# Kernel optimization log

Hardware: AMD Instinct MI355X
Metric: run time of the kernel (lower is better)

The kernel has to match this reference:

```python
import jax, jax.numpy as jnp
import numpy as np
from jax import lax

IN_CH = 192
CENTER_CH = 192
MID_CH = 192
K = 3
BS, H, W = 8, 64, 64
MASK_NUM = 16


def conv2d(x, w, b, padding=0, groups=1):
    # x: (N,C,H,W), w: (O, I/groups, kh, kw)
    out = lax.conv_general_dilated(
        x, w, window_strides=(1, 1),
        padding=[(padding, padding), (padding, padding)],
        dimension_numbers=('NCHW', 'OIHW', 'NCHW'),
        feature_group_count=groups)
    return out + b[None, :, None, None]


def lrelu(x):
    return jax.nn.leaky_relu(x, negative_slope=0.1)


def setup_inputs() -> dict:
    key = jax.random.key(0)
    ks = jax.random.split(key, 32)
    s = 0.02
    d = {
        'input': jax.random.normal(ks[0], (BS, IN_CH, H, W), jnp.float32),
        'list_center': jax.random.normal(ks[1], (BS, MASK_NUM, CENTER_CH), jnp.float32),
        'batch_mask': jax.random.randint(ks[2], (BS, H, W), 0, MASK_NUM),
        # self.conv: conv1x1(in,mid) -> lrelu -> conv1x1(mid,mid)
        'w0': jax.random.normal(ks[3], (MID_CH, IN_CH, 1, 1)) * s,
        'b0': jnp.zeros((MID_CH,)),
        'w1': jax.random.normal(ks[4], (MID_CH, MID_CH, 1, 1)) * s,
        'b1': jnp.zeros((MID_CH,)),
        # k_sp_gen: conv1x1(mid+center,mid), 3x3(mid,mid), depthwise 3x3(mid -> mid*k^2, groups=mid)
        'ws0': jax.random.normal(ks[5], (MID_CH, MID_CH + CENTER_CH, 1, 1)) * s,
        'bs0': jnp.zeros((MID_CH,)),
        'ws1': jax.random.normal(ks[6], (MID_CH, MID_CH, K, K)) * s,
        'bs1': jnp.zeros((MID_CH,)),
        'ws2': jax.random.normal(ks[7], (MID_CH * K * K, 1, K, K)) * s,
        'bs2': jnp.zeros((MID_CH * K * K,)),
        # k_ch_gen: GAP -> conv1x1 -> lrelu -> conv1x1 -> sigmoid
        'wc0': jax.random.normal(ks[8], (MID_CH, MID_CH, 1, 1)) * s,
        'bc0': jnp.zeros((MID_CH,)),
        'wc1': jax.random.normal(ks[9], (MID_CH, MID_CH, 1, 1)) * s,
        'bc1': jnp.zeros((MID_CH,)),
        # conv_out
        'wo': jax.random.normal(ks[10], (IN_CH, MID_CH, 1, 1)) * s,
        'bo': jnp.zeros((IN_CH,)),
    }
    return d


def mask_expand(list_center, batch_mask):
    # list_center: (bs, mask_num, ch); batch_mask: (bs, h, w) int
    # -> (bs, ch, h, w)
    gathered = jax.vmap(lambda c, m: c[m])(list_center, batch_mask)  # (bs,h,w,ch)
    return jnp.transpose(gathered, (0, 3, 1, 2))


def dynamic_conv(x, k_sp, k):
    # x: (bs, ch, h, w); k_sp: (bs, ch, k^2, h, w)
    bs, ch, h, w = x.shape
    p = (k - 1) // 2
    xp = jnp.pad(x, ((0, 0), (0, 0), (p, p), (p, p)))
    # torch Unfold ordering: kernel index = ki*k + kj, channel-major in view
    patches = jnp.stack([xp[:, :, i:i + h, j:j + w]
                         for i in range(k) for j in range(k)], axis=2)
    return jnp.einsum('bckhw,bckhw->bchw', patches, k_sp)


def reference(input, list_center, batch_mask, w0, b0, w1, b1, ws0, bs0,
              ws1, bs1, ws2, bs2, wc0, bc0, wc1, bc1, wo, bo):
    bs, _, h, w = input.shape
    k = K
    ch = MID_CH
    centers_exp = mask_expand(list_center, batch_mask)  # (bs, center_ch, h, w)
    shortcut = input
    x = conv2d(lrelu(conv2d(input, w0, b0)), w1, b1)  # self.conv
    y = jnp.concatenate([x, centers_exp], axis=1)
    y = lrelu(conv2d(y, ws0, bs0))
    y = lrelu(conv2d(y, ws1, bs1, padding=(k - 1) // 2))
    k_sp = conv2d(y, ws2, bs2, padding=(k - 1) // 2, groups=ch)
    k_sp = k_sp.reshape(bs, ch, k * k, h, w)
    out = dynamic_conv(x, k_sp, k)
    # squeeze-excite channel gate
    g = jnp.mean(out, axis=(2, 3), keepdims=True)
    g = jax.nn.sigmoid(conv2d(lrelu(conv2d(g, wc0, bc0)), wc1, bc1))
    out = g * out
    out = conv2d(out, wo, bo)
    return out + shortcut
```

## Files before the change

### kernel.cpp

```cpp
#include <hip/hip_runtime.h>
#include <hip/hip_bf16.h>

#define CH   192
#define PIX  4096
#define BSZ  8

using f32x4  = __attribute__((ext_vector_type(4))) float;
using short8 = __attribute__((ext_vector_type(8))) short;

__device__ __forceinline__ float bf2f(unsigned short u) {
    union { unsigned u32; float f; } x; x.u32 = ((unsigned)u) << 16; return x.f;
}
__device__ __forceinline__ unsigned short f2bf(float f) {
    union { float f; unsigned u; } x; x.f = f;
    unsigned u = x.u;
    unsigned r = (u + 0x7FFFu + ((u >> 16) & 1u)) >> 16;
    return (unsigned short)r;
}

__device__ __forceinline__ short8 ldsBs(const unsigned short* B, int ST, int k0, int px) {
    short8 f;
    #pragma unroll
    for (int e = 0; e < 8; ++e) f[e] = (short)B[(k0 + e) * ST + px];
    return f;
}

__global__ void k_prep_w(const float* __restrict__ w0, const float* __restrict__ w1,
                         const float* __restrict__ ws0, const float* __restrict__ wo,
                         const float* __restrict__ ws1,
                         unsigned short* __restrict__ w0f, unsigned short* __restrict__ w1f,
                         unsigned short* __restrict__ ws0xf, unsigned short* __restrict__ wof,
                         unsigned short* __restrict__ wc3f, float* __restrict__ gsum) {
    int i = blockIdx.x * 256 + threadIdx.x;
    if (i < 4*36864) {
        int which = i / 36864, j = i % 36864;
        int kc = j / 6144, r = j % 6144, mf = r / 512, r2 = r % 512;
        int l = r2 >> 3, e = r2 & 7;
        int o = mf*16 + (l & 15), k = kc*32 + ((l >> 4) << 3) + e;
        float v;
        unsigned short* dst;
        if (which == 0)      { v = w0[o*192 + k];  dst = w0f;   }
        else if (which == 1) { v = w1[o*192 + k];  dst = w1f;   }
        else if (which == 2) { v = ws0[o*384 + k]; dst = ws0xf; }
        else                 { v = wo[o*192 + k];  dst = wof;   }
        dst[j] = f2bf(v);
        return;
    }
    i -= 4*36864;
    if (i < 331776) {
        int tk = i / 6144, tap = tk / 6, kc = tk % 6;
        int r = i % 6144, mf = r / 512, r2 = r % 512;
        int l = r2 >> 3, e = r2 & 7;
        int o = mf*16 + (l & 15), c = kc*32 + ((l >> 4) << 3) + e;
        wc3f[i] = f2bf(ws1[(o*192 + c)*9 + tap]);
        return;
    }
    i -= 331776;
    if (i < 1536) gsum[i] = 0.f;
}

__global__ void k_tcent(const float* __restrict__ ws0, const float* __restrict__ lc,
                        float* __restrict__ tc) {
    int m = blockIdx.x, b = blockIdx.y, o = threadIdx.x;
    __shared__ float cbuf[192];
    cbuf[o] = lc[(b*16 + m)*192 + o];
    __syncthreads();
    float a = 0.f;
    const float* wr = ws0 + o*384 + 192;
    for (int c = 0; c < 192; ++c) a += wr[c] * cbuf[c];
    tc[(b*16 + m)*192 + o] = a;
}

__global__ __launch_bounds__(256) void k_fused3(
    const float* __restrict__ input,
    const unsigned short* __restrict__ w0f,
    const unsigned short* __restrict__ w1f,
    const unsigned short* __restrict__ ws0xf,
    const float* __restrict__ b0, const float* __restrict__ b1,
    const float* __restrict__ bs0,
    const float* __restrict__ tc, const int* __restrict__ mask,
    unsigned short* __restrict__ xg, unsigned short* __restrict__ y0t)
{
    const int b = blockIdx.y, n0 = blockIdx.x * 64;
    __shared__ unsigned short Bsm[192*66];
    __shared__ unsigned short Csm[192*67];
    const int tid = threadIdx.x, lane = tid & 63, wv = tid >> 6;
    const int li = lane & 15, kq = lane >> 4;

    {
        const float* src = input + (size_t)b*192*PIX + n0;
        #pragma unroll
        for (int j = 0; j < 6; ++j) {
            int q = tid + 256*j, k = q >> 3, g = (q & 7)*8;
            float4 v0 = *(const float4*)(src + (size_t)k*PIX + g);
            float4 v1 = *(const float4*)(src + (size_t)k*PIX + g + 4);
            unsigned d0 = f2bf(v0.x) | ((unsigned)f2bf(v0.y) << 16);
            unsigned d1 = f2bf(v0.z) | ((unsigned)f2bf(v0.w) << 16);
            unsigned d2 = f2bf(v1.x) | ((unsigned)f2bf(v1.y) << 16);
            unsigned d3 = f2bf(v1.z) | ((unsigned)f2bf(v1.w) << 16);
            unsigned* d = (unsigned*)(Bsm + k*66 + g);
            d[0]=d0; d[1]=d1; d[2]=d2; d[3]=d3;
        }
    }
    __syncthreads();

    f32x4 acc[3][4];

    #pragma unroll
    for (int m = 0; m < 3; ++m)
        #pragma unroll
        for (int n = 0; n < 4; ++n) acc[m][n] = {0.f,0.f,0.f,0.f};
    for (int kc = 0; kc < 6; ++kc) {
        short8 a[3];
        #pragma unroll
        for (int m = 0; m < 3; ++m)
            a[m] = *(const short8*)(w0f + ((kc*12 + wv*3 + m)*64 + lane)*8);
        #pragma unroll
        for (int n = 0; n < 4; ++n) {
            short8 fb = ldsBs(Bsm, 66, kc*32 + kq*8, n*16 + li);
            #pragma unroll
            for (int m = 0; m < 3; ++m)
                acc[m][n] = __builtin_amdgcn_mfma_f32_16x16x32_bf16(a[m], fb, acc[m][n], 0,0,0);
        }
    }
    #pragma unroll
    for (int m = 0; m < 3; ++m) {
        int o0 = (wv*3 + m)*16 + kq*4;
        #pragma unroll
        for (int n = 0; n < 4; ++n) {
            int px = n*16 + li;
            #pragma unroll
            for (int r = 0; r < 4; ++r) {
                float v = acc[m][n][r] + b0[o0 + r];
                v = v > 0.f ? v : 0.1f*v;
                Csm[(o0 + r)*67 + px] = f2bf(v);
            }
        }
    }
    __syncthreads();

    #pragma unroll
    for (int m = 0; m < 3; ++m)
        #pragma unroll
        for (int n = 0; n < 4; ++n) acc[m][n] = {0.f,0.f,0.f,0.f};
    for (int kc = 0; kc < 6; ++kc) {
        short8 a[3];
        #pragma unroll
        for (int m = 0; m < 3; ++m)
            a[m] = *(const short8*)(w1f + ((kc*12 + wv*3 + m)*64 + lane)*8);
        #pragma unroll
        for (int n = 0; n < 4; ++n) {
            short8 fb = ldsBs(Csm, 67, kc*32 + kq*8, n*16 + li);
            #pragma unroll
            for (int m = 0; m < 3; ++m)
                acc[m][n] = __builtin_amdgcn_mfma_f32_16x16x32_bf16(a[m], fb, acc[m][n], 0,0,0);
        }
    }
    __syncthreads();
    #pragma unroll
    for (int m = 0; m < 3; ++m) {
        int o0 = (wv*3 + m)*16 + kq*4;
        #pragma unroll
        for (int n = 0; n < 4; ++n) {
            int px = n*16 + li;
            #pragma unroll
            for (int r = 0; r < 4; ++r) {
                float v = acc[m][n][r] + b1[o0 + r];
                unsigned short h = f2bf(v);
                Bsm[(o0 + r)*66 + px] = h;
                xg[((size_t)b*192 + o0 + r)*PIX + n0 + px] = h;
            }
        }
    }
    __syncthreads();

    #pragma unroll
    for (int m = 0; m < 3; ++m)
        #pragma unroll
        for (int n = 0; n < 4; ++n) acc[m][n] = {0.f,0.f,0.f,0.f};
    for (int kc = 0; kc < 6; ++kc) {
        short8 a[3];
        #pragma unroll
        for (int m = 0; m < 3; ++m)
            a[m] = *(const short8*)(ws0xf + ((kc*12 + wv*3 + m)*64 + lane)*8);
        #pragma unroll
        for (int n = 0; n < 4; ++n) {
            short8 fb = ldsBs(Bsm, 66, kc*32 + kq*8, n*16 + li);
            #pragma unroll
            for (int m = 0; m < 3; ++m)
                acc[m][n] = __builtin_amdgcn_mfma_f32_16x16x32_bf16(a[m], fb, acc[m][n], 0,0,0);
        }
    }
    int mi_[4];
    #pragma unroll
    for (int n = 0; n < 4; ++n) mi_[n] = mask[b*PIX + n0 + n*16 + li];
    #pragma unroll
    for (int m = 0; m < 3; ++m) {
        int o0 = (wv*3 + m)*16 + kq*4;
        #pragma unroll
        for (int n = 0; n < 4; ++n) {
            int px = n*16 + li;
            const float* tcb = tc + (b*16 + mi_[n])*192;
            ushort4 w;
            unsigned short* wp = (unsigned short*)&w;
            #pragma unroll
            for (int r = 0; r < 4; ++r) {
                float v = acc[m][n][r] + bs0[o0 + r] + tcb[o0 + r];
                v = v > 0.f ? v : 0.1f*v;
                wp[r] = f2bf(v);
            }
            *(ushort4*)(Csm + px*200 + o0) = w;
        }
    }
    __syncthreads();
    #pragma unroll
    for (int j = 0; j < 6; ++j) {
        int u = tid + 256*j;
        int px = u / 24, chunk = u % 24;
        uint4 v = *(const uint4*)(Csm + px*200 + chunk*8);
        *(uint4*)(y0t + ((size_t)(b*4096 + n0 + px))*192 + chunk*8) = v;
    }
}

__global__ __launch_bounds__(512) void k_conv3t(
    const unsigned short* __restrict__ wc3f,
    const unsigned short* __restrict__ y0t,
    const float* __restrict__ bias,
    unsigned short* __restrict__ y1)
{
    const int b = blockIdx.y, h = blockIdx.x;
    __shared__ unsigned short Bs[3*66*40];
    const int tid = threadIdx.x, lane = tid & 63, wv = tid >> 6;
    const int li = lane & 15, kq = lane >> 4;
    const int mw = wv >> 1, nh = wv & 1;

    f32x4 acc[3][2];
    #pragma unroll
    for (int m = 0; m < 3; ++m)
        #pragma unroll
        for (int nn = 0; nn < 2; ++nn) acc[m][nn] = {0.f,0.f,0.f,0.f};

    for (int kc = 0; kc < 6; ++kc) {
        for (int u = tid; u < 792; u += 512) {
            int row = u >> 2, chunk = u & 3;
            int dr = row / 66, pxl = row % 66;
            int hh = h + dr - 1, pxg = pxl - 1;
            uint4 v = {0u,0u,0u,0u};
            if ((unsigned)hh < 64u && (unsigned)pxg < 64u)
                v = *(const uint4*)(y0t + ((size_t)(b*4096 + hh*64 + pxg))*192 + kc*32 + chunk*8);
            *(uint4*)((char*)Bs + row*80 + chunk*16) = v;
        }
        __syncthreads();

        #pragma unroll
        for (int tap = 0; tap < 9; ++tap) {
            const int dr = tap / 3, dc1 = tap % 3;
            short8 a[3];
            #pragma unroll
            for (int m = 0; m < 3; ++m)
                a[m] = *(const short8*)(wc3f + (((tap*6 + kc)*12 + mw*3 + m)*64 + lane)*8);
            #pragma unroll
            for (int nn = 0; nn < 2; ++nn) {
                int pxi = nh*32 + nn*16 + li + dc1;
                short8 fb = *(const short8*)((const char*)Bs + (dr*66 + pxi)*80 + kq*16);
                #pragma unroll
                for (int m = 0; m < 3; ++m)
                    acc[m][nn] = __builtin_amdgcn_mfma_f32_16x16x32_bf16(a[m], fb, acc[m][nn], 0,0,0);
            }
        }
        __syncthreads();
    }

    #pragma unroll
    for (int m = 0; m < 3; ++m) {
        int o0 = (mw*3 + m)*16 + kq*4;
        #pragma unroll
        for (int nn = 0; nn < 2; ++nn) {
            int px = h*64 + nh*32 + nn*16 + li;
            #pragma unroll
            for (int r = 0; r < 4; ++r) {
                float v = acc[m][nn][r] + bias[o0 + r];
                v = v > 0.f ? v : 0.1f*v;
                y1[((size_t)b*192 + o0 + r)*PIX + px] = f2bf(v);
            }
        }
    }
}

__global__ __launch_bounds__(256) void k_dwdyn2(
    const unsigned short* __restrict__ Y1,
    const unsigned short* __restrict__ X,
    const float* __restrict__ ws2,
    const float* __restrict__ bs2,
    unsigned short* __restrict__ OP,
    float* __restrict__ gsum)
{
    const int c = blockIdx.x, b = blockIdx.y;
    __shared__ unsigned short ysm[4096];
    __shared__ unsigned short xsm[4096];
    __shared__ float wsm[81], bsm9[9], red[4];
    const int tid = threadIdx.x;
    const size_t cb = ((size_t)b*192 + c) * PIX;
    #pragma unroll
    for (int j = 0; j < 2; ++j) {
        int i = tid + 256*j;
        *(uint4*)(ysm + i*8) = *(const uint4*)(Y1 + cb + i*8);
        *(uint4*)(xsm + i*8) = *(const uint4*)(X  + cb + i*8);
    }
    if (tid < 81) wsm[tid] = ws2[c*81 + tid];
    else if (tid < 90) bsm9[tid-81] = bs2[c*9 + tid - 81];
    __syncthreads();

    float gacc = 0.f;
    for (int i = 0; i < 16; ++i) {
        int px = tid + 256*i, hh = px >> 6, ww = px & 63;
        float ksp[9];
        #pragma unroll
        for (int j = 0; j < 9; ++j) ksp[j] = bsm9[j];
        #pragma unroll
        for (int tap = 0; tap < 9; ++tap) {
            int h2 = hh + tap/3 - 1, w2 = ww + tap%3 - 1;
            float yv = ((unsigned)h2 < 64u && (unsigned)w2 < 64u)
                       ? bf2f(ysm[h2*64 + w2]) : 0.f;
            #pragma unroll
            for (int j = 0; j < 9; ++j) ksp[j] += yv * wsm[j*9 + tap];
        }
        float out = 0.f;
        #pragma unroll
        for (int j = 0; j < 9; ++j) {
            int h2 = hh + j/3 - 1, w2 = ww + j%3 - 1;
            float xv = ((unsigned)h2 < 64u && (unsigned)w2 < 64u)
                       ? bf2f(xsm[h2*64 + w2]) : 0.f;
            out += xv * ksp[j];
        }
        OP[cb + px] = f2bf(out);
        gacc += out;
    }
    #pragma unroll
    for (int off = 32; off > 0; off >>= 1) gacc += __shfl_down(gacc, off);
    if ((tid & 63) == 0) red[tid >> 6] = gacc;
    __syncthreads();
    if (tid == 0) gsum[b*192 + c] = red[0] + red[1] + red[2] + red[3];
}

__global__ void k_gate(const float* __restrict__ gsum,
                       const float* __restrict__ wc0, const float* __restrict__ bc0,
                       const float* __restrict__ wc1, const float* __restrict__ bc1,
                       float* __restrict__ gvec)
{
    const int b = blockIdx.x, t = threadIdx.x;
    __shared__ float mean[192], s1[192];
    mean[t] = gsum[b*192 + t] * (1.f/4096.f);
    __syncthreads();
    float a = bc0[t];
    const float* w = wc0 + t*192;
    for (int i = 0; i < 192; ++i) a += w[i] * mean[i];
    s1[t] = a > 0.f ? a : 0.1f * a;
    __syncthreads();
    float a2 = bc1[t];
    const float* w2 = wc1 + t*192;
    for (int i = 0; i < 192; ++i) a2 += w2[i] * s1[i];
    gvec[b*192 + t] = 1.f / (1.f + __expf(-a2));
}

__global__ __launch_bounds__(256) void k_gemmo(
    const unsigned short* __restrict__ wof,
    const unsigned short* __restrict__ op,
    const float* __restrict__ bo,
    const float* __restrict__ gvec,
    const float* __restrict__ resid,
    float* __restrict__ out)
{
    const int b = blockIdx.y, n0 = blockIdx.x * 64;
    __shared__ unsigned short Bsm[192*66];
    const int tid = threadIdx.x, lane = tid & 63, wv = tid >> 6;
    const int li = lane & 15, kq = lane >> 4;

    {
        const unsigned short* src = op + (size_t)b*192*PIX + n0;
        #pragma unroll
        for (int j = 0; j < 6; ++j) {
            int q = tid + 256*j, k = q >> 3, g = (q & 7) * 8;
            uint4 v = *(const uint4*)(src + (size_t)k*PIX + g);
            float gs = gvec[b*192 + k];
            unsigned short* pv = (unsigned short*)&v;
            #pragma unroll
            for (int e = 0; e < 8; ++e) pv[e] = f2bf(bf2f(pv[e]) * gs);
            unsigned* d = (unsigned*)(Bsm + k*66 + g);
            const unsigned* s = (const unsigned*)&v;
            d[0]=s[0]; d[1]=s[1]; d[2]=s[2]; d[3]=s[3];
        }
    }
    __syncthreads();

    f32x4 acc[3][4];
    #pragma unroll
    for (int m = 0; m < 3; ++m)
        #pragma unroll
        for (int n = 0; n < 4; ++n) acc[m][n] = {0.f,0.f,0.f,0.f};
    for (int kc = 0; kc < 6; ++kc) {
        short8 a[3];
        #pragma unroll
        for (int m = 0; m < 3; ++m)
            a[m] = *(const short8*)(wof + ((kc*12 + wv*3 + m)*64 + lane)*8);
        #pragma unroll
        for (int n = 0; n < 4; ++n) {
            short8 fb = ldsBs(Bsm, 66, kc*32 + kq*8, n*16 + li);
            #pragma unroll
            for (int m = 0; m < 3; ++m)
                acc[m][n] = __builtin_amdgcn_mfma_f32_16x16x32_bf16(a[m], fb, acc[m][n], 0,0,0);
        }
    }
    #pragma unroll
    for (int m = 0; m < 3; ++m) {
        int o0 = (wv*3 + m)*16 + kq*4;
        #pragma unroll
        for (int n = 0; n < 4; ++n) {
            int px = n*16 + li;
            #pragma unroll
            for (int r = 0; r < 4; ++r) {
                size_t idx = ((size_t)b*192 + o0 + r)*PIX + n0 + px;
                out[idx] = acc[m][n][r] + bo[o0 + r] + resid[idx];
            }
        }
    }
}

extern "C" void kernel_launch(void* const* d_in, const int* in_sizes, int n_in,
                              void* d_out, int out_size, void* d_ws, size_t ws_size,
                              hipStream_t stream)
{
    const float* input = (const float*)d_in[0];
    const float* lc    = (const float*)d_in[1];
    const int*   mask  = (const int*)d_in[2];
    const float* w0  = (const float*)d_in[3];
    const float* b0  = (const float*)d_in[4];
    const float* w1  = (const float*)d_in[5];
    const float* b1  = (const float*)d_in[6];
    const float* ws0 = (const float*)d_in[7];
    const float* bs0 = (const float*)d_in[8];
    const float* ws1 = (const float*)d_in[9];
    const float* bs1 = (const float*)d_in[10];
    const float* ws2 = (const float*)d_in[11];
    const float* bs2 = (const float*)d_in[12];
    const float* wc0 = (const float*)d_in[13];
    const float* bc0 = (const float*)d_in[14];
    const float* wc1 = (const float*)d_in[15];
    const float* bc1 = (const float*)d_in[16];
    const float* wo  = (const float*)d_in[17];
    const float* bo  = (const float*)d_in[18];

    char* ws = (char*)d_ws;
    size_t off = 0;
    auto alloc = [&](size_t bytes) {
        void* p = ws + off; off = (off + bytes + 255) & ~(size_t)255; return p;
    };
    const size_t act_b = (size_t)BSZ * CH * PIX * 2;
    unsigned short* x_bf  = (unsigned short*)alloc(act_b);
    unsigned short* y0t   = (unsigned short*)alloc(act_b);
    unsigned short* y1_bf = (unsigned short*)alloc(act_b);
    unsigned short* op_bf = (unsigned short*)alloc(act_b);
    unsigned short* w0f   = (unsigned short*)alloc(36864*2);
    unsigned short* w1f   = (unsigned short*)alloc(36864*2);
    unsigned short* ws0xf = (unsigned short*)alloc(36864*2);
    unsigned short* wof   = (unsigned short*)alloc(36864*2);
    unsigned short* wc3f  = (unsigned short*)alloc(331776*2);
    float* tc   = (float*)alloc(8*16*192*4);
    float* gsum = (float*)alloc(1536*4);
    float* gvec = (float*)alloc(1536*4);

    k_prep_w<<<1878, 256, 0, stream>>>(w0, w1, ws0, wo, ws1, w0f, w1f, ws0xf, wof, wc3f, gsum);
    k_tcent<<<dim3(16, 8), 192, 0, stream>>>(ws0, lc, tc);

    dim3 gg(64, 8);
    k_fused3<<<gg, 256, 0, stream>>>(input, w0f, w1f, ws0xf, b0, b1, bs0, tc, mask, x_bf, y0t);
    k_conv3t<<<gg, 512, 0, stream>>>(wc3f, y0t, bs1, y1_bf);
    k_dwdyn2<<<dim3(192, 8), 256, 0, stream>>>(y1_bf, x_bf, ws2, bs2, op_bf, gsum);
    k_gate<<<8, 192, 0, stream>>>(gsum, wc0, bc0, wc1, bc1, gvec);
    k_gemmo<<<gg, 256, 0, stream>>>(wof, op_bf, bo, gvec, input, (float*)d_out);
}
```

Measured before the change: 232.2 us.

## Double-buffer conv3x3 loads, use a register sliding window in dwdyn, fold tcent into prep

```diff
diff --git a/kernel.cpp b/kernel.cpp
--- a/kernel.cpp
+++ b/kernel.cpp
@@ -27,10 +27,10 @@
 
 __global__ void k_prep_w(const float* __restrict__ w0, const float* __restrict__ w1,
                          const float* __restrict__ ws0, const float* __restrict__ wo,
-                         const float* __restrict__ ws1,
+                         const float* __restrict__ ws1, const float* __restrict__ lc,
                          unsigned short* __restrict__ w0f, unsigned short* __restrict__ w1f,
                          unsigned short* __restrict__ ws0xf, unsigned short* __restrict__ wof,
-                         unsigned short* __restrict__ wc3f, float* __restrict__ gsum) {
+                         unsigned short* __restrict__ wc3f, float* __restrict__ tc) {
     int i = blockIdx.x * 256 + threadIdx.x;
     if (i < 4*36864) {
         int which = i / 36864, j = i % 36864;
@@ -56,19 +56,14 @@
         return;
     }
     i -= 331776;
-    if (i < 1536) gsum[i] = 0.f;
-}
-
-__global__ void k_tcent(const float* __restrict__ ws0, const float* __restrict__ lc,
-                        float* __restrict__ tc) {
-    int m = blockIdx.x, b = blockIdx.y, o = threadIdx.x;
-    __shared__ float cbuf[192];
-    cbuf[o] = lc[(b*16 + m)*192 + o];
-    __syncthreads();
-    float a = 0.f;
-    const float* wr = ws0 + o*384 + 192;
-    for (int c = 0; c < 192; ++c) a += wr[c] * cbuf[c];
-    tc[(b*16 + m)*192 + o] = a;
+    if (i < 24576) {
+        int bm = i / 192, o = i % 192;
+        const float* wr = ws0 + o*384 + 192;
+        const float* cb = lc + bm*192;
+        float a = 0.f;
+        for (int c2 = 0; c2 < 192; ++c2) a += wr[c2] * cb[c2];
+        tc[i] = a;
+    }
 }
 
 __global__ __launch_bounds__(256) void k_fused3(
@@ -229,11 +224,32 @@
     unsigned short* __restrict__ y1)
 {
     const int b = blockIdx.y, h = blockIdx.x;
-    __shared__ unsigned short Bs[3*66*40];
+    __shared__ unsigned short Bs[2][3*66*40];
     const int tid = threadIdx.x, lane = tid & 63, wv = tid >> 6;
     const int li = lane & 15, kq = lane >> 4;
     const int mw = wv >> 1, nh = wv & 1;
 
+    const int u1 = tid + 512;
+    const int r0 = tid >> 2,  c0 = tid & 3;
+    const int dr0 = r0/66, px0g = r0%66 - 1, hh0 = h + dr0 - 1;
+    const bool ok0 = ((unsigned)hh0 < 64u) & ((unsigned)px0g < 64u);
+    const size_t s0 = ok0 ? ((size_t)(b*4096 + hh0*64 + px0g))*192 + c0*8 : 0;
+    const int o0f = r0*80 + c0*16;
+    const int r1 = u1 >> 2,  c1 = u1 & 3;
+    const int dr1 = r1/66, px1g = r1%66 - 1, hh1 = h + dr1 - 1;
+    const bool act1 = (u1 < 792);
+    const bool ok1 = act1 & ((unsigned)hh1 < 64u) & ((unsigned)px1g < 64u);
+    const size_t s1 = ok1 ? ((size_t)(b*4096 + hh1*64 + px1g))*192 + c1*8 : 0;
+    const int o1f = r1*80 + c1*16;
+    const uint4 zz = {0u,0u,0u,0u};
+
+    uint4 v0, v1;
+    v0 = ok0 ? *(const uint4*)(y0t + s0) : zz;
+    v1 = ok1 ? *(const uint4*)(y0t + s1) : zz;
+    *(uint4*)((char*)Bs[0] + o0f) = v0;
+    if (act1) *(uint4*)((char*)Bs[0] + o1f) = v1;
+    __syncthreads();
+
     f32x4 acc[3][2];
     #pragma unroll
     for (int m = 0; m < 3; ++m)
@@ -241,17 +257,12 @@
         for (int nn = 0; nn < 2; ++nn) acc[m][nn] = {0.f,0.f,0.f,0.f};
 
     for (int kc = 0; kc < 6; ++kc) {
-        for (int u = tid; u < 792; u += 512) {
-            int row = u >> 2, chunk = u & 3;
-            int dr = row / 66, pxl = row % 66;
-            int hh = h + dr - 1, pxg = pxl - 1;
-            uint4 v = {0u,0u,0u,0u};
-            if ((unsigned)hh < 64u && (unsigned)pxg < 64u)
-                v = *(const uint4*)(y0t + ((size_t)(b*4096 + hh*64 + pxg))*192 + kc*32 + chunk*8);
-            *(uint4*)((char*)Bs + row*80 + chunk*16) = v;
-        }
-        __syncthreads();
-
+        const int cur = kc & 1;
+        if (kc < 5) {
+            v0 = ok0 ? *(const uint4*)(y0t + s0 + (kc+1)*32) : zz;
+            v1 = ok1 ? *(const uint4*)(y0t + s1 + (kc+1)*32) : zz;
+        }
+        const unsigned short* Bc = Bs[cur];
         #pragma unroll
         for (int tap = 0; tap < 9; ++tap) {
             const int dr = tap / 3, dc1 = tap % 3;
@@ -262,32 +273,36 @@
             #pragma unroll
             for (int nn = 0; nn < 2; ++nn) {
                 int pxi = nh*32 + nn*16 + li + dc1;
-                short8 fb = *(const short8*)((const char*)Bs + (dr*66 + pxi)*80 + kq*16);
+                short8 fb = *(const short8*)((const char*)Bc + (dr*66 + pxi)*80 + kq*16);
                 #pragma unroll
                 for (int m = 0; m < 3; ++m)
                     acc[m][nn] = __builtin_amdgcn_mfma_f32_16x16x32_bf16(a[m], fb, acc[m][nn], 0,0,0);
             }
         }
-        __syncthreads();
+        if (kc < 5) {
+            *(uint4*)((char*)Bs[cur^1] + o0f) = v0;
+            if (act1) *(uint4*)((char*)Bs[cur^1] + o1f) = v1;
+            __syncthreads();
+        }
     }
 
     #pragma unroll
     for (int m = 0; m < 3; ++m) {
-        int o0 = (mw*3 + m)*16 + kq*4;
+        int oo = (mw*3 + m)*16 + kq*4;
         #pragma unroll
         for (int nn = 0; nn < 2; ++nn) {
             int px = h*64 + nh*32 + nn*16 + li;
             #pragma unroll
             for (int r = 0; r < 4; ++r) {
-                float v = acc[m][nn][r] + bias[o0 + r];
+                float v = acc[m][nn][r] + bias[oo + r];
                 v = v > 0.f ? v : 0.1f*v;
-                y1[((size_t)b*192 + o0 + r)*PIX + px] = f2bf(v);
+                y1[((size_t)b*192 + oo + r)*PIX + px] = f2bf(v);
             }
         }
     }
 }
 
-__global__ __launch_bounds__(256) void k_dwdyn2(
+__global__ __launch_bounds__(256) void k_dwdyn3(
     const unsigned short* __restrict__ Y1,
     const unsigned short* __restrict__ X,
     const float* __restrict__ ws2,
@@ -298,7 +313,7 @@
     const int c = blockIdx.x, b = blockIdx.y;
     __shared__ unsigned short ysm[4096];
     __shared__ unsigned short xsm[4096];
-    __shared__ float wsm[81], bsm9[9], red[4];
+    __shared__ float red[4];
     const int tid = threadIdx.x;
     const size_t cb = ((size_t)b*192 + c) * PIX;
     #pragma unroll
@@ -307,34 +322,67 @@
         *(uint4*)(ysm + i*8) = *(const uint4*)(Y1 + cb + i*8);
         *(uint4*)(xsm + i*8) = *(const uint4*)(X  + cb + i*8);
     }
-    if (tid < 81) wsm[tid] = ws2[c*81 + tid];
-    else if (tid < 90) bsm9[tid-81] = bs2[c*9 + tid - 81];
-    __syncthreads();
+    float wreg[81], breg[9];
+    #pragma unroll
+    for (int t = 0; t < 81; ++t) wreg[t] = ws2[c*81 + t];
+    #pragma unroll
+    for (int t = 0; t < 9; ++t) breg[t] = bs2[c*9 + t];
+    __syncthreads();
+
+    const int w = tid & 63, rg = tid >> 6, h0 = rg * 16;
+    const bool wl = (w > 0), wr = (w < 63);
+
+    float ya[3], yb[3], yc[3], xa[3], xb[3], xc[3];
+    {
+        int h = h0 - 1;
+        if (h >= 0) {
+            int base = h*64 + w;
+            ya[0] = wl ? bf2f(ysm[base-1]) : 0.f;  ya[1] = bf2f(ysm[base]);
+            ya[2] = wr ? bf2f(ysm[base+1]) : 0.f;
+            xa[0] = wl ? bf2f(xsm[base-1]) : 0.f;  xa[1] = bf2f(xsm[base]);
+            xa[2] = wr ? bf2f(xsm[base+1]) : 0.f;
+        } else { ya[0]=ya[1]=ya[2]=0.f; xa[0]=xa[1]=xa[2]=0.f; }
+        int base = h0*64 + w;
+        yb[0] = wl ? bf2f(ysm[base-1]) : 0.f;  yb[1] = bf2f(ysm[base]);
+        yb[2] = wr ? bf2f(ysm[base+1]) : 0.f;
+        xb[0] = wl ? bf2f(xsm[base-1]) : 0.f;  xb[1] = bf2f(xsm[base]);
+        xb[2] = wr ? bf2f(xsm[base+1]) : 0.f;
+    }
 
     float gacc = 0.f;
-    for (int i = 0; i < 16; ++i) {
-        int px = tid + 256*i, hh = px >> 6, ww = px & 63;
+    #pragma unroll 4
+    for (int j = 0; j < 16; ++j) {
+        int h = h0 + j;
+        if (h + 1 < 64) {
+            int base = (h+1)*64 + w;
+            yc[0] = wl ? bf2f(ysm[base-1]) : 0.f;  yc[1] = bf2f(ysm[base]);
+            yc[2] = wr ? bf2f(ysm[base+1]) : 0.f;
+            xc[0] = wl ? bf2f(xsm[base-1]) : 0.f;  xc[1] = bf2f(xsm[base]);
+            xc[2] = wr ? bf2f(xsm[base+1]) : 0.f;
+        } else { yc[0]=yc[1]=yc[2]=0.f; xc[0]=xc[1]=xc[2]=0.f; }
+
         float ksp[9];
         #pragma unroll
-        for (int j = 0; j < 9; ++j) ksp[j] = bsm9[j];
-        #pragma unroll
-        for (int tap = 0; tap < 9; ++tap) {
-            int h2 = hh + tap/3 - 1, w2 = ww + tap%3 - 1;
-            float yv = ((unsigned)h2 < 64u && (unsigned)w2 < 64u)
-                       ? bf2f(ysm[h2*64 + w2]) : 0.f;
-            #pragma unroll
-            for (int j = 0; j < 9; ++j) ksp[j] += yv * wsm[j*9 + tap];
-        }
-        float out = 0.f;
-        #pragma unroll
-        for (int j = 0; j < 9; ++j) {
-            int h2 = hh + j/3 - 1, w2 = ww + j%3 - 1;
-            float xv = ((unsigned)h2 < 64u && (unsigned)w2 < 64u)
-                       ? bf2f(xsm[h2*64 + w2]) : 0.f;
-            out += xv * ksp[j];
-        }
-        OP[cb + px] = f2bf(out);
+        for (int t = 0; t < 9; ++t) ksp[t] = breg[t];
+        #pragma unroll
+        for (int tj = 0; tj < 3; ++tj) {
+            #pragma unroll
+            for (int t = 0; t < 9; ++t) ksp[t] += ya[tj] * wreg[t*9 + tj];
+            #pragma unroll
+            for (int t = 0; t < 9; ++t) ksp[t] += yb[tj] * wreg[t*9 + 3 + tj];
+            #pragma unroll
+            for (int t = 0; t < 9; ++t) ksp[t] += yc[tj] * wreg[t*9 + 6 + tj];
+        }
+        float out = xa[0]*ksp[0] + xa[1]*ksp[1] + xa[2]*ksp[2]
+                  + xb[0]*ksp[3] + xb[1]*ksp[4] + xb[2]*ksp[5]
+                  + xc[0]*ksp[6] + xc[1]*ksp[7] + xc[2]*ksp[8];
+        OP[cb + h*64 + w] = f2bf(out);
         gacc += out;
+        #pragma unroll
+        for (int t = 0; t < 3; ++t) {
+            ya[t] = yb[t]; yb[t] = yc[t];
+            xa[t] = xb[t]; xb[t] = xc[t];
+        }
     }
     #pragma unroll
     for (int off = 32; off > 0; off >>= 1) gacc += __shfl_down(gacc, off);
@@ -469,13 +517,13 @@
     float* gsum = (float*)alloc(1536*4);
     float* gvec = (float*)alloc(1536*4);
 
-    k_prep_w<<<1878, 256, 0, stream>>>(w0, w1, ws0, wo, ws1, w0f, w1f, ws0xf, wof, wc3f, gsum);
-    k_tcent<<<dim3(16, 8), 192, 0, stream>>>(ws0, lc, tc);
+    k_prep_w<<<1968, 256, 0, stream>>>(w0, w1, ws0, wo, ws1, lc,
+                                       w0f, w1f, ws0xf, wof, wc3f, tc);
 
     dim3 gg(64, 8);
     k_fused3<<<gg, 256, 0, stream>>>(input, w0f, w1f, ws0xf, b0, b1, bs0, tc, mask, x_bf, y0t);
     k_conv3t<<<gg, 512, 0, stream>>>(wc3f, y0t, bs1, y1_bf);
-    k_dwdyn2<<<dim3(192, 8), 256, 0, stream>>>(y1_bf, x_bf, ws2, bs2, op_bf, gsum);
+    k_dwdyn3<<<dim3(192, 8), 256, 0, stream>>>(y1_bf, x_bf, ws2, bs2, op_bf, gsum);
     k_gate<<<8, 192, 0, stream>>>(gsum, wc0, bc0, wc1, bc1, gvec);
     k_gemmo<<<gg, 256, 0, stream>>>(wof, op_bf, bo, gvec, input, (float*)d_out);
 }
```

After: 229.2 us. About the same (-1.3%).
